# Performance work log

Hardware: AMD Instinct MI355X
Metric: run time of the kernel (lower is better)

## Reference

```python
import jax, jax.numpy as jnp
import numpy as np

N_NODES = 10000
N_EDGES = 100000
IN_CH = 64
EDGE_DIM = 16
HID = 128
HEADS = 4
LAYERS = 4
NUM_GRAPHS = 256


def setup_inputs() -> dict:
    key = jax.random.key(0)
    ks = jax.random.split(key, 16)
    s = 0.1
    HC = HEADS * HID
    L = LAYERS
    return {
        "x": jax.random.normal(ks[0], (N_NODES, IN_CH), jnp.float32),
        "edge_index": jax.random.randint(ks[1], (2, N_EDGES), 0, N_NODES, dtype=jnp.int32),
        "edge_attr": jax.random.normal(ks[2], (N_EDGES, EDGE_DIM), jnp.float32),
        "batch": jnp.sort(jax.random.randint(ks[3], (N_NODES,), 0, NUM_GRAPHS, dtype=jnp.int32)),
        "Win": jax.random.normal(ks[4], (IN_CH, HID), jnp.float32) * s,
        "b_in": jnp.zeros((HID,), jnp.float32),
        "Wl": jax.random.normal(ks[5], (L, HID, HC), jnp.float32) * s,
        "bl": jnp.zeros((L, HC), jnp.float32),
        "Wr": jax.random.normal(ks[6], (L, HID, HC), jnp.float32) * s,
        "br": jnp.zeros((L, HC), jnp.float32),
        "We": jax.random.normal(ks[7], (L, EDGE_DIM, HC), jnp.float32) * s,
        "att": jax.random.normal(ks[8], (L, HEADS, HID), jnp.float32) * s,
        "b_gat": jnp.zeros((L, HID), jnp.float32),
        "gamma": jnp.ones((L, HID), jnp.float32),
        "beta": jnp.zeros((L, HID), jnp.float32),
        "Wres": jax.random.normal(ks[9], (L - 1, HID, HID), jnp.float32) * s,
        "bres": jnp.zeros((L - 1, HID), jnp.float32),
        "W1": jax.random.normal(ks[10], (HID, HID), jnp.float32) * s,
        "b1": jnp.zeros((HID,), jnp.float32),
        "W2": jax.random.normal(ks[11], (HID, HID // 2), jnp.float32) * s,
        "b2": jnp.zeros((HID // 2,), jnp.float32),
        "W3": jax.random.normal(ks[12], (HID // 2, 1), jnp.float32) * s,
        "b3": jnp.zeros((1,), jnp.float32),
    }


def _layer_norm(x, g, b):
    mu = x.mean(-1, keepdims=True)
    var = ((x - mu) ** 2).mean(-1, keepdims=True)
    return g * (x - mu) / jnp.sqrt(var + 1e-5) + b


def _gatv2(h, src, dst, edge_attr, Wl, bl, Wr, br, We, att, bias):
    # GATv2Conv, concat=False, share_weights=False, negative_slope=0.2, eval mode
    N = h.shape[0]
    H, C = att.shape
    xl = (h @ Wl + bl).reshape(N, H, C)   # source-side features (lin_l)
    xr = (h @ Wr + br).reshape(N, H, C)   # target-side features (lin_r)
    e = (edge_attr @ We).reshape(-1, H, C)
    m = xl[src] + xr[dst] + e             # [E, H, C]
    m = jnp.where(m > 0, m, 0.2 * m)      # leaky_relu
    logits = jnp.einsum('ehc,hc->eh', m, att)
    lmax = jax.lax.stop_gradient(jax.ops.segment_max(logits, dst, num_segments=N))
    p = jnp.exp(logits - lmax[dst])
    denom = jax.ops.segment_sum(p, dst, num_segments=N)
    alpha = p / (denom[dst] + 1e-16)      # segment softmax over in-edges of each target
    out = jax.ops.segment_sum(alpha[:, :, None] * xl[src], dst, num_segments=N)
    return out.mean(axis=1) + bias        # concat=False -> head mean, plus bias


def reference(x, edge_index, edge_attr, batch, Win, b_in, Wl, bl, Wr, br, We, att,
              b_gat, gamma, beta, Wres, bres, W1, b1, W2, b2, W3, b3):
    src, dst = edge_index[0], edge_index[1]
    h = jax.nn.elu(x @ Win + b_in)
    for i in range(LAYERS):
        h_res = h
        h = _gatv2(h, src, dst, edge_attr, Wl[i], bl[i], Wr[i], br[i], We[i], att[i], b_gat[i])
        h = jax.nn.elu(_layer_norm(h, gamma[i], beta[i]))
        if i > 0:
            h = h + (h_res @ Wres[i - 1] + bres[i - 1])
    sums = jax.ops.segment_sum(h, batch, num_segments=NUM_GRAPHS)
    counts = jax.ops.segment_sum(jnp.ones((h.shape[0], 1), h.dtype), batch, num_segments=NUM_GRAPHS)
    hg = sums / jnp.maximum(counts, 1.0)  # global_mean_pool
    z = jax.nn.relu(hg @ W1 + b1)
    z = jax.nn.relu(z @ W2 + b2)
    return (z @ W3 + b3).reshape(-1)
```

## Files before the change

### kernel.cpp

```cpp
#include <hip/hip_runtime.h>

#define N_NODES 10000
#define N_EDGES 100000
#define IN_CH 64
#define EDGE_DIM 16
#define HID 128
#define HEADS 4
#define HC 512
#define LAYERS 4
#define NUM_GRAPHS 256
#define NCAT 1152
#define LDPK 72

#define PREP_BLOCKS 320
#define DEG_BLOCKS 782

typedef __bf16 bf16;
typedef __bf16 bf16x8 __attribute__((ext_vector_type(8)));
typedef __bf16 bf16x4 __attribute__((ext_vector_type(4)));
typedef float floatx4 __attribute__((ext_vector_type(4)));
typedef _Float16 f16;
typedef _Float16 f16x2 __attribute__((ext_vector_type(2)));

__device__ __forceinline__ float elu_f(float x) { return x > 0.f ? x : (__expf(x) - 1.f); }

__global__ __launch_bounds__(128) void k_prep_all(
    const float* __restrict__ Wl, const float* __restrict__ bl,
    const float* __restrict__ Wr, const float* __restrict__ br,
    const float* __restrict__ Wres, const float* __restrict__ bres,
    const float* __restrict__ We,
    bf16* __restrict__ WT, float* __restrict__ bcat, f16* __restrict__ WeH,
    const int* __restrict__ ei, const int* __restrict__ batch,
    int* __restrict__ deg, int* __restrict__ cnt,
    const float* __restrict__ x, const float* __restrict__ Win,
    const float* __restrict__ b_in, bf16* __restrict__ h_bf) {
    __shared__ float smem[16 * 129];
    int b = blockIdx.x;
    int t = threadIdx.x;

    if (b < PREP_BLOCKS) {
        int nt = b % 10, i = (b / 10) % LAYERS, z = b / 40;
        if (nt == 9) {
            if (z < 4) {
                int c = z * 128 + t;
                const float* src = We + (size_t)i * EDGE_DIM * HC + c;
                f16 buf[16];
#pragma unroll
                for (int k = 0; k < EDGE_DIM; k++) buf[k] = (f16)src[(size_t)k * HC];
                f16* dst = WeH + ((size_t)i * HC + c) * EDGE_DIM;
                *(uint4*)dst = *(uint4*)buf;
                *(uint4*)(dst + 8) = *(uint4*)(buf + 8);
            }
            return;
        }
        float (*tile)[129] = (float(*)[129])smem;
        int n0 = nt * 128;
        const float* base = nullptr; const float* bsrc = nullptr; int ld = 0;
        if (nt < 4)       { base = Wl + (size_t)i * HID * HC + n0;          bsrc = bl + i * HC + n0;              ld = HC; }
        else if (nt < 8)  { base = Wr + (size_t)i * HID * HC + (n0 - 512);  bsrc = br + i * HC + (n0 - 512);      ld = HC; }
        else if (i > 0)   { base = Wres + (size_t)(i - 1) * HID * HID;      bsrc = bres + (size_t)(i - 1) * HID;  ld = HID; }
        if (base) {
#pragma unroll
            for (int r = 0; r < 16; r++) tile[r][t] = base[(size_t)(z * 16 + r) * ld + t];
        } else {
#pragma unroll
            for (int r = 0; r < 16; r++) tile[r][t] = 0.f;
        }
        __syncthreads();
        int n = n0 + t;
        if (z == 0) bcat[(size_t)i * NCAT + n] = base ? bsrc[t] : 0.f;
        bf16* dst = WT + ((size_t)i * NCAT + n) * HID + z * 16;
#pragma unroll
        for (int kc = 0; kc < 2; kc++) {
            bf16x8 v;
#pragma unroll
            for (int u = 0; u < 8; u++) v[u] = (bf16)tile[kc * 8 + u][t];
            *(bf16x8*)(dst + kc * 8) = v;
        }
    } else if (b < PREP_BLOCKS + DEG_BLOCKS) {
        int e = (b - PREP_BLOCKS) * 128 + t;
        if (e < N_EDGES) atomicAdd(&deg[ei[N_EDGES + e]], 1);
        if (e < N_NODES) atomicAdd(&cnt[batch[e]], 1);
    } else {
        int n = b - (PREP_BLOCKS + DEG_BLOCKS);
        float* xs = smem;
        if (t < IN_CH) xs[t] = x[(size_t)n * IN_CH + t];
        __syncthreads();
        float s = b_in[t];
#pragma unroll 8
        for (int k = 0; k < IN_CH; k++) s = fmaf(xs[k], Win[k * HID + t], s);
        h_bf[(size_t)n * HID + t] = (bf16)elu_f(s);
    }
}

__global__ __launch_bounds__(256) void k_gemm_mfma(
    const bf16* __restrict__ A, const bf16* __restrict__ WT,
    const float* __restrict__ bcat, bf16* __restrict__ C, int M) {
    __shared__ __align__(16) unsigned short As[128 * LDPK];
    __shared__ __align__(16) unsigned short Bs[128 * LDPK];
    int t = threadIdx.x;
    int r0 = blockIdx.x * 128, c0 = blockIdx.y * 128;

    int wave = t >> 6, lane = t & 63;
    int wm = wave & 1, wn = wave >> 1;
    int quad = lane >> 4, lm = lane & 15;
    floatx4 zero = {0.f, 0.f, 0.f, 0.f};
    floatx4 acc[4][4];
#pragma unroll
    for (int mi = 0; mi < 4; mi++)
#pragma unroll
        for (int ni = 0; ni < 4; ni++) acc[mi][ni] = zero;

    const unsigned short* Ab = &As[(wm * 64 + lm) * LDPK + quad * 8];
    const unsigned short* Bb = &Bs[(wn * 64 + lm) * LDPK + quad * 8];

    for (int kc = 0; kc < 2; kc++) {
#pragma unroll
        for (int i = 0; i < 4; i++) {
            int idx = t + i * 256;
            int row = idx >> 3;
            int ch = idx & 7;
            int r = r0 + row; if (r >= M) r = M - 1;
            *(uint4*)&As[row * LDPK + ch * 8] =
                *(const uint4*)(A + (size_t)r * HID + kc * 64 + ch * 8);
            *(uint4*)&Bs[row * LDPK + ch * 8] =
                *(const uint4*)(WT + (size_t)(c0 + row) * HID + kc * 64 + ch * 8);
        }
        __syncthreads();
#pragma unroll
        for (int ks = 0; ks < 2; ks++) {
            bf16x8 af[4], bfr[4];
#pragma unroll
            for (int mi = 0; mi < 4; mi++) af[mi] = *(const bf16x8*)(Ab + mi * 16 * LDPK + ks * 32);
#pragma unroll
            for (int ni = 0; ni < 4; ni++) bfr[ni] = *(const bf16x8*)(Bb + ni * 16 * LDPK + ks * 32);
#pragma unroll
            for (int mi = 0; mi < 4; mi++)
#pragma unroll
                for (int ni = 0; ni < 4; ni++)
                    acc[mi][ni] = __builtin_amdgcn_mfma_f32_16x16x32_bf16(bfr[ni], af[mi], acc[mi][ni], 0, 0, 0);
        }
        __syncthreads();
    }

#pragma unroll
    for (int mi = 0; mi < 4; mi++) {
        int row = r0 + wm * 64 + mi * 16 + lm;
        if (row < M) {
            bf16* crow = C + (size_t)row * NCAT;
#pragma unroll
            for (int ni = 0; ni < 4; ni++) {
                int cb = c0 + wn * 64 + ni * 16 + quad * 4;
                float4 b4 = *(const float4*)(bcat + cb);
                floatx4 v = acc[mi][ni];
                bf16x4 o = {(bf16)(v[0] + b4.x), (bf16)(v[1] + b4.y),
                            (bf16)(v[2] + b4.z), (bf16)(v[3] + b4.w)};
                *(bf16x4*)(crow + cb) = o;
            }
        }
    }
}

__global__ __launch_bounds__(1024) void k_scan(const int* __restrict__ deg,
                                               int* __restrict__ row_start,
                                               int* __restrict__ cursor,
                                               int* __restrict__ order) {
    __shared__ int wsum[16];
    __shared__ int carry_s;
    __shared__ int hist[64];
    __shared__ int binoff[64];
    int t = threadIdx.x;
    int wave = t >> 6, lane = t & 63;
    if (t == 0) { carry_s = 0; row_start[0] = 0; }
    __syncthreads();
    for (int base = 0; base < N_NODES; base += 4096) {
        int i0 = base + t * 4;
        int v[4];
#pragma unroll
        for (int u = 0; u < 4; u++) v[u] = (i0 + u < N_NODES) ? deg[i0 + u] : 0;
        int tsum = v[0] + v[1] + v[2] + v[3];
        int incl = tsum;
#pragma unroll
        for (int off = 1; off < 64; off <<= 1) {
            int u = __shfl_up(incl, off, 64);
            if (lane >= off) incl += u;
        }
        if (lane == 63) wsum[wave] = incl;
        __syncthreads();
        if (wave == 0) {
            int ws = (lane < 16) ? wsum[lane] : 0;
#pragma unroll
            for (int off = 1; off < 16; off <<= 1) {
                int u = __shfl_up(ws, off, 64);
                if (lane >= off) ws += u;
            }
            if (lane < 16) wsum[lane] = ws;
        }
        __syncthreads();
        int carry = carry_s;
        int chunk_total = wsum[15];
        int p = carry + ((wave == 0) ? 0 : wsum[wave - 1]) + incl - tsum;
#pragma unroll
        for (int u = 0; u < 4; u++) {
            int i = i0 + u;
            if (i < N_NODES) { cursor[i] = p; p += v[u]; row_start[i + 1] = p; }
        }
        __syncthreads();
        if (t == 0) carry_s = carry + chunk_total;
    }

    if (t < 64) hist[t] = 0;
    __syncthreads();
    for (int i = t; i < N_NODES; i += 1024) {
        int d = deg[i]; if (d > 63) d = 63;
        atomicAdd(&hist[d], 1);
    }
    __syncthreads();
    if (t < 64) {
        int s = hist[t];
#pragma unroll
        for (int off = 1; off < 64; off <<= 1) {
            int u = __shfl_down(s, off, 64);
            if (t + off >= 64) u = 0;
            s += u;
        }
        binoff[t] = s - hist[t];
    }
    __syncthreads();
    for (int i = t; i < N_NODES; i += 1024) {
        int d = deg[i]; if (d > 63) d = 63;
        int pos = atomicAdd(&binoff[d], 1);
        order[pos] = i;
    }
}

__global__ void k_scatter(const int* __restrict__ ei, const float* __restrict__ edge_attr,
                          int* __restrict__ cursor,
                          int* __restrict__ ssrc, f16* __restrict__ ea_h) {
    int e = blockIdx.x * blockDim.x + threadIdx.x;
    if (e < N_EDGES) {
        int d = ei[N_EDGES + e];
        int pos = atomicAdd(&cursor[d], 1);
        ssrc[pos] = ei[e];
        const float* s = edge_attr + (size_t)e * EDGE_DIM;
        f16 buf[16];
#pragma unroll
        for (int q = 0; q < 16; q++) buf[q] = (f16)s[q];
        f16* dst = ea_h + (size_t)pos * EDGE_DIM;
        *(uint4*)dst = *(uint4*)buf;
        *(uint4*)(dst + 8) = *(uint4*)(buf + 8);
    }
}

__global__ __launch_bounds__(128) void k_edge_fused(
    const bf16* __restrict__ xlr, const f16* __restrict__ ea_h,
    const int* __restrict__ row_start, const int* __restrict__ ssrc,
    const int* __restrict__ order,
    const f16* __restrict__ WeH_l, const float* __restrict__ att_l,
    const float* __restrict__ bgat_l, const float* __restrict__ gamma_l,
    const float* __restrict__ beta_l,
    int has_res,
    const int* __restrict__ batch, float* __restrict__ hsum, int do_pool,
    bf16* __restrict__ hbf_out) {
    int n = order[blockIdx.x];
    int t = threadIdx.x;
    int wave = t >> 6;
    int lane = t & 63;
    int c0 = wave * 256 + lane * 4;
    int head = c0 >> 7;

    const f16x2* wr = (const f16x2*)(WeH_l + (size_t)c0 * EDGE_DIM);
    float4 att4 = *(const float4*)(att_l + head * HID + (c0 & 127));
    bf16x4 vr = *(const bf16x4*)(xlr + (size_t)n * NCAT + 512 + c0);
    float xr0 = (float)vr[0], xr1 = (float)vr[1], xr2 = (float)vr[2], xr3 = (float)vr[3];

    int e0 = row_start[n], e1 = row_start[n + 1];
    float l0 = 0.f, l1 = 0.f;
    float4 a0 = {0.f, 0.f, 0.f, 0.f}, a1 = {0.f, 0.f, 0.f, 0.f};

    int j = e0;
    for (; j + 1 < e1; j += 2) {
        int s0 = ssrc[j], s1 = ssrc[j + 1];
        const f16x2* eah = (const f16x2*)(ea_h + (size_t)j * EDGE_DIM);
        f16x2 ep0[8], ep1[8];
#pragma unroll
        for (int kp = 0; kp < 8; kp++) ep0[kp] = eah[kp];
#pragma unroll
        for (int kp = 0; kp < 8; kp++) ep1[kp] = eah[8 + kp];
        bf16x4 vl0 = *(const bf16x4*)(xlr + (size_t)s0 * NCAT + c0);
        bf16x4 vl1 = *(const bf16x4*)(xlr + (size_t)s1 * NCAT + c0);

        float p0c0 = 0.f, p0c1 = 0.f, p0c2 = 0.f, p0c3 = 0.f;
        float p1c0 = 0.f, p1c1 = 0.f, p1c2 = 0.f, p1c3 = 0.f;
#pragma unroll
        for (int kp = 0; kp < 8; kp++) {
            p0c0 = __builtin_amdgcn_fdot2(wr[kp],      ep0[kp], p0c0, false);
            p1c0 = __builtin_amdgcn_fdot2(wr[kp],      ep1[kp], p1c0, false);
            p0c1 = __builtin_amdgcn_fdot2(wr[8 + kp],  ep0[kp], p0c1, false);
            p1c1 = __builtin_amdgcn_fdot2(wr[8 + kp],  ep1[kp], p1c1, false);
            p0c2 = __builtin_amdgcn_fdot2(wr[16 + kp], ep0[kp], p0c2, false);
            p1c2 = __builtin_amdgcn_fdot2(wr[16 + kp], ep1[kp], p1c2, false);
            p0c3 = __builtin_amdgcn_fdot2(wr[24 + kp], ep0[kp], p0c3, false);
            p1c3 = __builtin_amdgcn_fdot2(wr[24 + kp], ep1[kp], p1c3, false);
        }
        float x00 = (float)vl0[0], x01 = (float)vl0[1], x02 = (float)vl0[2], x03 = (float)vl0[3];
        float x10 = (float)vl1[0], x11 = (float)vl1[1], x12 = (float)vl1[2], x13 = (float)vl1[3];
        float m00 = x00 + xr0 + p0c0; m00 = fmaxf(m00, 0.2f * m00);
        float m01 = x01 + xr1 + p0c1; m01 = fmaxf(m01, 0.2f * m01);
        float m02 = x02 + xr2 + p0c2; m02 = fmaxf(m02, 0.2f * m02);
        float m03 = x03 + xr3 + p0c3; m03 = fmaxf(m03, 0.2f * m03);
        float m10 = x10 + xr0 + p1c0; m10 = fmaxf(m10, 0.2f * m10);
        float m11 = x11 + xr1 + p1c1; m11 = fmaxf(m11, 0.2f * m11);
        float m12 = x12 + xr2 + p1c2; m12 = fmaxf(m12, 0.2f * m12);
        float m13 = x13 + xr3 + p1c3; m13 = fmaxf(m13, 0.2f * m13);
        float part0 = m00 * att4.x + m01 * att4.y + m02 * att4.z + m03 * att4.w;
        float part1 = m10 * att4.x + m11 * att4.y + m12 * att4.z + m13 * att4.w;
#pragma unroll
        for (int off = 1; off < 32; off <<= 1) {
            part0 += __shfl_xor(part0, off, 64);
            part1 += __shfl_xor(part1, off, 64);
        }
        float p0 = __expf(part0);
        float p1 = __expf(part1);
        l0 += p0; l1 += p1;
        a0.x = fmaf(p0, x00, a0.x); a0.y = fmaf(p0, x01, a0.y);
        a0.z = fmaf(p0, x02, a0.z); a0.w = fmaf(p0, x03, a0.w);
        a1.x = fmaf(p1, x10, a1.x); a1.y = fmaf(p1, x11, a1.y);
        a1.z = fmaf(p1, x12, a1.z); a1.w = fmaf(p1, x13, a1.w);
    }
    if (j < e1) {
        int s0 = ssrc[j];
        const f16x2* eah = (const f16x2*)(ea_h + (size_t)j * EDGE_DIM);
        f16x2 ep0[8];
#pragma unroll
        for (int kp = 0; kp < 8; kp++) ep0[kp] = eah[kp];
        bf16x4 vl0 = *(const bf16x4*)(xlr + (size_t)s0 * NCAT + c0);
        float p0c0 = 0.f, p0c1 = 0.f, p0c2 = 0.f, p0c3 = 0.f;
#pragma unroll
        for (int kp = 0; kp < 8; kp++) {
            p0c0 = __builtin_amdgcn_fdot2(wr[kp],      ep0[kp], p0c0, false);
            p0c1 = __builtin_amdgcn_fdot2(wr[8 + kp],  ep0[kp], p0c1, false);
            p0c2 = __builtin_amdgcn_fdot2(wr[16 + kp], ep0[kp], p0c2, false);
            p0c3 = __builtin_amdgcn_fdot2(wr[24 + kp], ep0[kp], p0c3, false);
        }
        float x00 = (float)vl0[0], x01 = (float)vl0[1], x02 = (float)vl0[2], x03 = (float)vl0[3];
        float m00 = x00 + xr0 + p0c0; m00 = fmaxf(m00, 0.2f * m00);
        float m01 = x01 + xr1 + p0c1; m01 = fmaxf(m01, 0.2f * m01);
        float m02 = x02 + xr2 + p0c2; m02 = fmaxf(m02, 0.2f * m02);
        float m03 = x03 + xr3 + p0c3; m03 = fmaxf(m03, 0.2f * m03);
        float part0 = m00 * att4.x + m01 * att4.y + m02 * att4.z + m03 * att4.w;
#pragma unroll
        for (int off = 1; off < 32; off <<= 1) part0 += __shfl_xor(part0, off, 64);
        float p0 = __expf(part0);
        l0 += p0;
        a0.x = fmaf(p0, x00, a0.x); a0.y = fmaf(p0, x01, a0.y);
        a0.z = fmaf(p0, x02, a0.z); a0.w = fmaf(p0, x03, a0.w);
    }

    float inv = 1.f / (l0 + l1 + 1e-16f);

    __shared__ float sout[HC];
    __shared__ float red[4];
    sout[c0 + 0] = (a0.x + a1.x) * inv;
    sout[c0 + 1] = (a0.y + a1.y) * inv;
    sout[c0 + 2] = (a0.z + a1.z) * inv;
    sout[c0 + 3] = (a0.w + a1.w) * inv;
    __syncthreads();

    int c = t;
    float v = 0.25f * (sout[c] + sout[c + 128] + sout[c + 256] + sout[c + 384]) + bgat_l[c];
    float s1 = v, s2 = v * v;
#pragma unroll
    for (int off = 1; off < 64; off <<= 1) {
        s1 += __shfl_xor(s1, off, 64);
        s2 += __shfl_xor(s2, off, 64);
    }
    if (lane == 0) { red[wave * 2] = s1; red[wave * 2 + 1] = s2; }
    __syncthreads();
    s1 = red[0] + red[2];
    s2 = red[1] + red[3];
    float mu = s1 * (1.f / HID);
    float var = s2 * (1.f / HID) - mu * mu;
    float rstd = rsqrtf(var + 1e-5f);
    float y = fmaf(gamma_l[c] * (v - mu), rstd, beta_l[c]);
    y = elu_f(y);
    if (has_res) y += (float)xlr[(size_t)n * NCAT + 1024 + c];
    if (do_pool) atomicAdd(&hsum[(size_t)batch[n] * HID + c], y);
    else hbf_out[(size_t)n * HID + c] = (bf16)y;
}

__global__ __launch_bounds__(128) void k_mlp(const float* __restrict__ hsum,
                                             const int* __restrict__ cnt,
                                             const float* __restrict__ W1, const float* __restrict__ b1,
                                             const float* __restrict__ W2, const float* __restrict__ b2,
                                             const float* __restrict__ W3, const float* __restrict__ b3,
                                             float* __restrict__ out) {
    int g = blockIdx.x, t = threadIdx.x;
    __shared__ float hg[HID], z1[HID], z2[64];
    float invc = 1.f / fmaxf((float)cnt[g], 1.f);
    hg[t] = hsum[(size_t)g * HID + t] * invc;
    __syncthreads();
    float s = b1[t];
#pragma unroll 8
    for (int k = 0; k < HID; k++) s = fmaf(hg[k], W1[k * HID + t], s);
    z1[t] = fmaxf(s, 0.f);
    __syncthreads();
    if (t < 64) {
        float s2 = b2[t];
#pragma unroll 8
        for (int k = 0; k < HID; k++) s2 = fmaf(z1[k], W2[k * 64 + t], s2);
        z2[t] = fmaxf(s2, 0.f);
    }
    __syncthreads();
    if (t < 64) {
        float s3 = z2[t] * W3[t];
#pragma unroll
        for (int off = 1; off < 64; off <<= 1) s3 += __shfl_xor(s3, off, 64);
        if (t == 0) out[g] = s3 + b3[0];
    }
}

extern "C" void kernel_launch(void* const* d_in, const int* in_sizes, int n_in,
                              void* d_out, int out_size, void* d_ws, size_t ws_size,
                              hipStream_t stream) {
    const float* x         = (const float*)d_in[0];
    const int*   ei        = (const int*)  d_in[1];
    const float* edge_attr = (const float*)d_in[2];
    const int*   batch     = (const int*)  d_in[3];
    const float* Win       = (const float*)d_in[4];
    const float* b_in      = (const float*)d_in[5];
    const float* Wl        = (const float*)d_in[6];
    const float* bl        = (const float*)d_in[7];
    const float* Wr        = (const float*)d_in[8];
    const float* br        = (const float*)d_in[9];
    const float* We        = (const float*)d_in[10];
    const float* att       = (const float*)d_in[11];
    const float* b_gat     = (const float*)d_in[12];
    const float* gamma     = (const float*)d_in[13];
    const float* beta      = (const float*)d_in[14];
    const float* Wres      = (const float*)d_in[15];
    const float* bres      = (const float*)d_in[16];
    const float* W1        = (const float*)d_in[17];
    const float* b1        = (const float*)d_in[18];
    const float* W2        = (const float*)d_in[19];
    const float* b2        = (const float*)d_in[20];
    const float* W3        = (const float*)d_in[21];
    const float* b3        = (const float*)d_in[22];
    float* out = (float*)d_out;

    char* ws = (char*)d_ws;
    size_t off = 0;
    auto alloc = [&](size_t bytes) -> void* {
        void* p = ws + off;
        off = (off + bytes + 255) & ~(size_t)255;
        return p;
    };
    bf16*  h_bf    = (bf16*) alloc((size_t)N_NODES * HID * 2);
    bf16*  xlr     = (bf16*) alloc((size_t)N_NODES * NCAT * 2);
    bf16*  WT      = (bf16*) alloc((size_t)LAYERS * NCAT * HID * 2);
    float* bcat    = (float*)alloc((size_t)LAYERS * NCAT * 4);
    f16*   WeH     = (f16*)  alloc((size_t)LAYERS * HC * EDGE_DIM * 2);
    f16*   ea_h    = (f16*)  alloc((size_t)N_EDGES * EDGE_DIM * 2);
    char*  zbase   = ws + off;
    float* hsum    = (float*)alloc((size_t)NUM_GRAPHS * HID * 4);
    int*   cnt     = (int*)  alloc((size_t)NUM_GRAPHS * 4);
    int*   deg     = (int*)  alloc((size_t)N_NODES * 4);
    size_t zlen    = (size_t)((ws + off) - zbase);
    int*   rowst   = (int*)  alloc((size_t)(N_NODES + 1) * 4);
    int*   cursor  = (int*)  alloc((size_t)N_NODES * 4);
    int*   ssrc    = (int*)  alloc((size_t)N_EDGES * 4);
    int*   order   = (int*)  alloc((size_t)N_NODES * 4);
    (void)ws_size;

    hipMemsetAsync(zbase, 0, zlen, stream);

    k_prep_all<<<PREP_BLOCKS + DEG_BLOCKS + N_NODES, 128, 0, stream>>>(
        Wl, bl, Wr, br, Wres, bres, We, WT, bcat, WeH,
        ei, batch, deg, cnt, x, Win, b_in, h_bf);
    k_scan<<<1, 1024, 0, stream>>>(deg, rowst, cursor, order);
    k_scatter<<<(N_EDGES + 255) / 256, 256, 0, stream>>>(ei, edge_attr, cursor, ssrc, ea_h);

    const int MG = (N_NODES + 127) / 128;
    for (int i = 0; i < LAYERS; i++) {
        int ntiles = (i > 0) ? (NCAT / 128) : (1024 / 128);
        k_gemm_mfma<<<dim3(MG, ntiles), 256, 0, stream>>>(
            h_bf, WT + (size_t)i * NCAT * HID, bcat + (size_t)i * NCAT, xlr, N_NODES);
        k_edge_fused<<<N_NODES, 128, 0, stream>>>(
            xlr, ea_h, rowst, ssrc, order,
            WeH + (size_t)i * HC * EDGE_DIM, att + (size_t)i * HEADS * HID,
            b_gat + (size_t)i * HID, gamma + (size_t)i * HID, beta + (size_t)i * HID,
            (i > 0) ? 1 : 0,
            batch, hsum, (i == LAYERS - 1) ? 1 : 0, h_bf);
    }

    k_mlp<<<NUM_GRAPHS, 128, 0, stream>>>(hsum, cnt, W1, b1, W2, b2, W3, b3, out);
}
```

Measured before the change: 407.8 us.

## Split edges across waves with eight channels per lane in GATv2 edge kernel

Each lane now covers eight channels, so one wave spans all four heads. The two waves of a block take interleaved in-edges instead of splitting the channels, and each wave keeps two independent accumulator chains. Partial sums and per-head softmax denominators from both waves are merged through shared memory. This halves the serial edge loop per wave and shortens the attention shuffle reduction, at the cost of more registers per lane and an extra shared-memory merge.

```diff
diff --git a/kernel.cpp b/kernel.cpp
--- a/kernel.cpp
+++ b/kernel.cpp
@@ -252,6 +252,37 @@
     }
 }
 
+__device__ __forceinline__ void edge_body8(
+    int j, const int* __restrict__ ssrc, const f16* __restrict__ ea_h,
+    const bf16* __restrict__ xlr, int c0, const f16x2* __restrict__ wr,
+    const float* xr, const float* attc, float& lsum, float* acc) {
+    int s = ssrc[j];
+    const f16x2* eah = (const f16x2*)(ea_h + (size_t)j * EDGE_DIM);
+    f16x2 ep[8];
+#pragma unroll
+    for (int kp = 0; kp < 8; kp++) ep[kp] = eah[kp];
+    bf16x8 vl = *(const bf16x8*)(xlr + (size_t)s * NCAT + c0);
+    float part = 0.f;
+    float x[8];
+#pragma unroll
+    for (int c = 0; c < 8; c++) {
+        float ec = 0.f;
+#pragma unroll
+        for (int kp = 0; kp < 8; kp++)
+            ec = __builtin_amdgcn_fdot2(wr[c * 8 + kp], ep[kp], ec, false);
+        x[c] = (float)vl[c];
+        float m = x[c] + xr[c] + ec;
+        m = fmaxf(m, 0.2f * m);
+        part = fmaf(m, attc[c], part);
+    }
+#pragma unroll
+    for (int off = 1; off < 16; off <<= 1) part += __shfl_xor(part, off, 64);
+    float p = __expf(part);
+    lsum += p;
+#pragma unroll
+    for (int c = 0; c < 8; c++) acc[c] = fmaf(p, x[c], acc[c]);
+}
+
 __global__ __launch_bounds__(128) void k_edge_fused(
     const bf16* __restrict__ xlr, const f16* __restrict__ ea_h,
     const int* __restrict__ row_start, const int* __restrict__ ssrc,
@@ -262,113 +293,62 @@
     int has_res,
     const int* __restrict__ batch, float* __restrict__ hsum, int do_pool,
     bf16* __restrict__ hbf_out) {
-    int n = order[blockIdx.x];
     int t = threadIdx.x;
     int wave = t >> 6;
     int lane = t & 63;
-    int c0 = wave * 256 + lane * 4;
-    int head = c0 >> 7;
+    int n = order[blockIdx.x];
+    int c0 = lane * 8;
+    int head = lane >> 4;
+    int ca = (lane & 15) * 8;
 
     const f16x2* wr = (const f16x2*)(WeH_l + (size_t)c0 * EDGE_DIM);
-    float4 att4 = *(const float4*)(att_l + head * HID + (c0 & 127));
-    bf16x4 vr = *(const bf16x4*)(xlr + (size_t)n * NCAT + 512 + c0);
-    float xr0 = (float)vr[0], xr1 = (float)vr[1], xr2 = (float)vr[2], xr3 = (float)vr[3];
+    float attc[8], xr[8];
+    {
+        float4 aA = *(const float4*)(att_l + head * HID + ca);
+        float4 aB = *(const float4*)(att_l + head * HID + ca + 4);
+        attc[0] = aA.x; attc[1] = aA.y; attc[2] = aA.z; attc[3] = aA.w;
+        attc[4] = aB.x; attc[5] = aB.y; attc[6] = aB.z; attc[7] = aB.w;
+        bf16x8 vr8 = *(const bf16x8*)(xlr + (size_t)n * NCAT + 512 + c0);
+#pragma unroll
+        for (int c = 0; c < 8; c++) xr[c] = (float)vr8[c];
+    }
 
     int e0 = row_start[n], e1 = row_start[n + 1];
-    float l0 = 0.f, l1 = 0.f;
-    float4 a0 = {0.f, 0.f, 0.f, 0.f}, a1 = {0.f, 0.f, 0.f, 0.f};
-
-    int j = e0;
-    for (; j + 1 < e1; j += 2) {
-        int s0 = ssrc[j], s1 = ssrc[j + 1];
-        const f16x2* eah = (const f16x2*)(ea_h + (size_t)j * EDGE_DIM);
-        f16x2 ep0[8], ep1[8];
-#pragma unroll
-        for (int kp = 0; kp < 8; kp++) ep0[kp] = eah[kp];
-#pragma unroll
-        for (int kp = 0; kp < 8; kp++) ep1[kp] = eah[8 + kp];
-        bf16x4 vl0 = *(const bf16x4*)(xlr + (size_t)s0 * NCAT + c0);
-        bf16x4 vl1 = *(const bf16x4*)(xlr + (size_t)s1 * NCAT + c0);
-
-        float p0c0 = 0.f, p0c1 = 0.f, p0c2 = 0.f, p0c3 = 0.f;
-        float p1c0 = 0.f, p1c1 = 0.f, p1c2 = 0.f, p1c3 = 0.f;
-#pragma unroll
-        for (int kp = 0; kp < 8; kp++) {
-            p0c0 = __builtin_amdgcn_fdot2(wr[kp],      ep0[kp], p0c0, false);
-            p1c0 = __builtin_amdgcn_fdot2(wr[kp],      ep1[kp], p1c0, false);
-            p0c1 = __builtin_amdgcn_fdot2(wr[8 + kp],  ep0[kp], p0c1, false);
-            p1c1 = __builtin_amdgcn_fdot2(wr[8 + kp],  ep1[kp], p1c1, false);
-            p0c2 = __builtin_amdgcn_fdot2(wr[16 + kp], ep0[kp], p0c2, false);
-            p1c2 = __builtin_amdgcn_fdot2(wr[16 + kp], ep1[kp], p1c2, false);
-            p0c3 = __builtin_amdgcn_fdot2(wr[24 + kp], ep0[kp], p0c3, false);
-            p1c3 = __builtin_amdgcn_fdot2(wr[24 + kp], ep1[kp], p1c3, false);
-        }
-        float x00 = (float)vl0[0], x01 = (float)vl0[1], x02 = (float)vl0[2], x03 = (float)vl0[3];
-        float x10 = (float)vl1[0], x11 = (float)vl1[1], x12 = (float)vl1[2], x13 = (float)vl1[3];
-        float m00 = x00 + xr0 + p0c0; m00 = fmaxf(m00, 0.2f * m00);
-        float m01 = x01 + xr1 + p0c1; m01 = fmaxf(m01, 0.2f * m01);
-        float m02 = x02 + xr2 + p0c2; m02 = fmaxf(m02, 0.2f * m02);
-        float m03 = x03 + xr3 + p0c3; m03 = fmaxf(m03, 0.2f * m03);
-        float m10 = x10 + xr0 + p1c0; m10 = fmaxf(m10, 0.2f * m10);
-        float m11 = x11 + xr1 + p1c1; m11 = fmaxf(m11, 0.2f * m11);
-        float m12 = x12 + xr2 + p1c2; m12 = fmaxf(m12, 0.2f * m12);
-        float m13 = x13 + xr3 + p1c3; m13 = fmaxf(m13, 0.2f * m13);
-        float part0 = m00 * att4.x + m01 * att4.y + m02 * att4.z + m03 * att4.w;
-        float part1 = m10 * att4.x + m11 * att4.y + m12 * att4.z + m13 * att4.w;
-#pragma unroll
-        for (int off = 1; off < 32; off <<= 1) {
-            part0 += __shfl_xor(part0, off, 64);
-            part1 += __shfl_xor(part1, off, 64);
-        }
-        float p0 = __expf(part0);
-        float p1 = __expf(part1);
-        l0 += p0; l1 += p1;
-        a0.x = fmaf(p0, x00, a0.x); a0.y = fmaf(p0, x01, a0.y);
-        a0.z = fmaf(p0, x02, a0.z); a0.w = fmaf(p0, x03, a0.w);
-        a1.x = fmaf(p1, x10, a1.x); a1.y = fmaf(p1, x11, a1.y);
-        a1.z = fmaf(p1, x12, a1.z); a1.w = fmaf(p1, x13, a1.w);
-    }
-    if (j < e1) {
-        int s0 = ssrc[j];
-        const f16x2* eah = (const f16x2*)(ea_h + (size_t)j * EDGE_DIM);
-        f16x2 ep0[8];
-#pragma unroll
-        for (int kp = 0; kp < 8; kp++) ep0[kp] = eah[kp];
-        bf16x4 vl0 = *(const bf16x4*)(xlr + (size_t)s0 * NCAT + c0);
-        float p0c0 = 0.f, p0c1 = 0.f, p0c2 = 0.f, p0c3 = 0.f;
-#pragma unroll
-        for (int kp = 0; kp < 8; kp++) {
-            p0c0 = __builtin_amdgcn_fdot2(wr[kp],      ep0[kp], p0c0, false);
-            p0c1 = __builtin_amdgcn_fdot2(wr[8 + kp],  ep0[kp], p0c1, false);
-            p0c2 = __builtin_amdgcn_fdot2(wr[16 + kp], ep0[kp], p0c2, false);
-            p0c3 = __builtin_amdgcn_fdot2(wr[24 + kp], ep0[kp], p0c3, false);
-        }
-        float x00 = (float)vl0[0], x01 = (float)vl0[1], x02 = (float)vl0[2], x03 = (float)vl0[3];
-        float m00 = x00 + xr0 + p0c0; m00 = fmaxf(m00, 0.2f * m00);
-        float m01 = x01 + xr1 + p0c1; m01 = fmaxf(m01, 0.2f * m01);
-        float m02 = x02 + xr2 + p0c2; m02 = fmaxf(m02, 0.2f * m02);
-        float m03 = x03 + xr3 + p0c3; m03 = fmaxf(m03, 0.2f * m03);
-        float part0 = m00 * att4.x + m01 * att4.y + m02 * att4.z + m03 * att4.w;
-#pragma unroll
-        for (int off = 1; off < 32; off <<= 1) part0 += __shfl_xor(part0, off, 64);
-        float p0 = __expf(part0);
-        l0 += p0;
-        a0.x = fmaf(p0, x00, a0.x); a0.y = fmaf(p0, x01, a0.y);
-        a0.z = fmaf(p0, x02, a0.z); a0.w = fmaf(p0, x03, a0.w);
-    }
-
-    float inv = 1.f / (l0 + l1 + 1e-16f);
-
-    __shared__ float sout[HC];
+    float lA = 0.f, lB = 0.f;
+    float aA8[8], aB8[8];
+#pragma unroll
+    for (int c = 0; c < 8; c++) { aA8[c] = 0.f; aB8[c] = 0.f; }
+
+    int j = e0 + wave;
+    for (; j + 2 < e1; j += 4) {
+        edge_body8(j,     ssrc, ea_h, xlr, c0, wr, xr, attc, lA, aA8);
+        edge_body8(j + 2, ssrc, ea_h, xlr, c0, wr, xr, attc, lB, aB8);
+    }
+    if (j < e1)
+        edge_body8(j,     ssrc, ea_h, xlr, c0, wr, xr, attc, lA, aA8);
+
+    __shared__ float sacc[2][HC];
+    __shared__ float sl[2][HEADS];
     __shared__ float red[4];
-    sout[c0 + 0] = (a0.x + a1.x) * inv;
-    sout[c0 + 1] = (a0.y + a1.y) * inv;
-    sout[c0 + 2] = (a0.z + a1.z) * inv;
-    sout[c0 + 3] = (a0.w + a1.w) * inv;
+    {
+        floatx4 o0 = {aA8[0] + aB8[0], aA8[1] + aB8[1], aA8[2] + aB8[2], aA8[3] + aB8[3]};
+        floatx4 o1 = {aA8[4] + aB8[4], aA8[5] + aB8[5], aA8[6] + aB8[6], aA8[7] + aB8[7]};
+        *(floatx4*)&sacc[wave][c0] = o0;
+        *(floatx4*)&sacc[wave][c0 + 4] = o1;
+        if ((lane & 15) == 0) sl[wave][head] = lA + lB;
+    }
     __syncthreads();
 
     int c = t;
-    float v = 0.25f * (sout[c] + sout[c + 128] + sout[c + 256] + sout[c + 384]) + bgat_l[c];
+    float v = 0.f;
+#pragma unroll
+    for (int h = 0; h < HEADS; h++) {
+        float lt = sl[0][h] + sl[1][h];
+        float invh = 1.f / (lt + 1e-16f);
+        v += (sacc[0][h * HID + c] + sacc[1][h * HID + c]) * invh;
+    }
+    v = 0.25f * v + bgat_l[c];
+
     float s1 = v, s2 = v * v;
 #pragma unroll
     for (int off = 1; off < 64; off <<= 1) {
```

After: 529.7 us. +29.9%, slower.
